# Optimization experiments

Hardware: AMD Instinct MI355X
Metric: run time of the kernel (lower is better)

## Reference

```python
import jax, jax.numpy as jnp
import numpy as np

N, Tq, Tk = 4096, 48, 48
E, H = 64, 4
HD = E // H
TN = 288            # time_num (5-min slots per day)
FE = 4              # forward_expansion
EPS = 1e-5


def _ln(x, g, b):
    mu = jnp.mean(x, axis=-1, keepdims=True)
    var = jnp.var(x, axis=-1, keepdims=True)
    return (x - mu) * jax.lax.rsqrt(var + EPS) * g + b


def setup_inputs() -> dict:
    rng = jax.random.key(0)
    ks = jax.random.split(rng, 12)
    s = 0.05
    return {
        "value": jax.random.normal(ks[0], (N, Tk, E), jnp.float32),
        "keys": jax.random.normal(ks[1], (N, Tk, E), jnp.float32),
        "query": jax.random.normal(ks[2], (N, Tq, E), jnp.float32),
        "Wv": jax.random.normal(ks[3], (HD, HD), jnp.float32) * s,
        "Wk": jax.random.normal(ks[4], (HD, HD), jnp.float32) * s,
        "Wq": jax.random.normal(ks[5], (HD, HD), jnp.float32) * s,
        "Wo": jax.random.normal(ks[6], (E, E), jnp.float32) * s,
        "bo": jnp.zeros((E,), jnp.float32),
        "temb": jax.random.normal(ks[7], (TN, E), jnp.float32) * s,
        "ln1_g": jnp.ones((E,), jnp.float32),
        "ln1_b": jnp.zeros((E,), jnp.float32),
        "ln2_g": jnp.ones((E,), jnp.float32),
        "ln2_b": jnp.zeros((E,), jnp.float32),
        "W1": jax.random.normal(ks[8], (FE * E, E), jnp.float32) * s,  # torch Linear(E, FE*E).weight
        "b1": jnp.zeros((FE * E,), jnp.float32),
        "W2": jax.random.normal(ks[9], (E, FE * E), jnp.float32) * s,
        "b2": jnp.zeros((E,), jnp.float32),
        "tq": 10,
    }


def reference(value, keys, query, Wv, Wk, Wq, Wo, bo, temb,
              ln1_g, ln1_b, ln2_g, ln2_b, W1, b1, W2, b2, tq):
    # temporal embedding add (tk = tq since tk=-1 default)
    tq_inds = (TN + tq + jnp.arange(Tq)) % TN
    tk_inds = (TN + tq + jnp.arange(Tk)) % TN
    q = query + temb[tq_inds][None, :, :]   # (N,Tq,E)
    k = keys + temb[tk_inds][None, :, :]    # (N,Tk,E)

    qh = q.reshape(N, Tq, H, HD)
    kh = k.reshape(N, Tk, H, HD)
    vh = value.reshape(N, Tk, H, HD)
    # per-head small linear projections (x @ W.T, no bias)
    qh = jnp.einsum('nthd,ed->nthe', qh, Wq)
    kh = jnp.einsum('nthd,ed->nthe', kh, Wk)
    vh = jnp.einsum('nthd,ed->nthe', vh, Wv)

    energy = jnp.einsum('nqhd,nkhd->nqkh', qh, kh)  # (N,Tq,Tk,H)
    # causal mask (mask=True path): masked entries set to -1e6 BEFORE scale+clamp
    tmask = jnp.tril(jnp.ones((Tq, Tk), jnp.float32))
    energy = jnp.where(tmask[None, :, :, None] == 0, jnp.float32(-1e6), energy)
    logits = jnp.clip(energy / jnp.float32(np.sqrt(E)), -5.0, 5.0)
    attention = jax.nn.softmax(logits, axis=2)       # softmax over k

    out = jnp.einsum('nqkh,nkhd->nqhd', attention, vh).reshape(N, Tq, E)
    out = out @ Wo.T + bo

    x = _ln(out + q, ln1_g, ln1_b)                   # dropout is identity (eval)
    ff = jax.nn.relu(x @ W1.T + b1) @ W2.T + b2
    return _ln(ff + x, ln2_g, ln2_b)
```

## Files before the change

kernel.cpp:

```cpp
#include <hip/hip_runtime.h>
#include <hip/hip_bf16.h>
#include <math.h>

#define NSEQ 4096
#define TN 288
#define EPSF 1e-5f

typedef short bf16x8 __attribute__((ext_vector_type(8)));
typedef float f32x4 __attribute__((ext_vector_type(4)));

#define WSV 0
#define WSK 256
#define WSQ 512
#define WSO 768
#define WS1 4864
#define WS2 21248

#define A_S   0
#define B_S   3456
#define C_S   6912
#define D_S   10496
#define CD_F  3456
#define H_S   6912

__device__ __forceinline__ unsigned short f2bf_u(float f) {
    __hip_bfloat16 h = __float2bfloat16(f);
    return *reinterpret_cast<const unsigned short*>(&h);
}
__device__ __forceinline__ unsigned int pk2(float a, float b) {
    return (unsigned int)f2bf_u(a) | ((unsigned int)f2bf_u(b) << 16);
}
__device__ __forceinline__ float bits2f(unsigned int u) { return __uint_as_float(u); }
__device__ __forceinline__ float halfsum(float v) {
    v += __shfl_xor(v, 1);
    v += __shfl_xor(v, 2);
    v += __shfl_xor(v, 4);
    v += __shfl_xor(v, 8);
    v += __shfl_xor(v, 16);
    return v;
}

__global__ void wconv_kernel(const float* __restrict__ Wv, const float* __restrict__ Wk,
                             const float* __restrict__ Wq, const float* __restrict__ Wo,
                             const float* __restrict__ W1, const float* __restrict__ W2,
                             short* __restrict__ ws) {
    int i = blockIdx.x * 256 + threadIdx.x;
    float v;
    if (i < 256)        v = Wv[i];
    else if (i < 512)   v = Wk[i - 256];
    else if (i < 768)   v = Wq[i - 512] * 0.125f;
    else if (i < 4864)  v = Wo[i - 768];
    else if (i < 21248) v = W1[i - 4864];
    else                v = W2[i - 21248];
    ws[i] = (short)f2bf_u(v);
}

__global__ __launch_bounds__(256, 5)
void ttrans_kernel(const float* __restrict__ value,
                   const float* __restrict__ keys,
                   const float* __restrict__ query,
                   const float* __restrict__ bo,
                   const float* __restrict__ temb,
                   const float* __restrict__ ln1g,
                   const float* __restrict__ ln1b,
                   const float* __restrict__ ln2g,
                   const float* __restrict__ ln2b,
                   const float* __restrict__ pb1,
                   const float* __restrict__ pb2,
                   const short* __restrict__ ws,
                   const int* __restrict__ tqp,
                   float* __restrict__ out)
{
    __shared__ __align__(16) unsigned char smem[27136];
    short* S16 = reinterpret_cast<short*>(smem);
    float* S32 = reinterpret_cast<float*>(smem);

    const int tid  = threadIdx.x;
    const int lane = tid & 63;
    const int w    = tid >> 6;
    const int l15  = lane & 15;
    const int lg   = lane >> 4;
    const int n    = blockIdx.x;
    const size_t gbase = (size_t)n * 3072;
    const int tqv  = *tqp;
    const int c0   = (lane & 31) * 2;
    const int sub  = lane >> 5;
    const int hh   = w;

    float2 qres2[6];
    {
        int t0 = w * 12 + sub;
        int ti = ((tqv % TN) + TN + t0) % TN;
        #pragma unroll
        for (int it2 = 0; it2 < 6; ++it2) {
            int t = t0 + it2 * 2;
            float2 tv = *reinterpret_cast<const float2*>(&temb[ti * 64 + c0]);
            float2 qv = *reinterpret_cast<const float2*>(&query[gbase + t * 64 + c0]);
            float2 kv = *reinterpret_cast<const float2*>(&keys [gbase + t * 64 + c0]);
            float2 vv = *reinterpret_cast<const float2*>(&value[gbase + t * 64 + c0]);
            float q0 = qv.x + tv.x, q1 = qv.y + tv.y;
            float k0 = kv.x + tv.x, k1 = kv.y + tv.y;
            qres2[it2] = make_float2(q0, q1);
            *reinterpret_cast<unsigned int*>(&S16[A_S + t * 72 + c0]) = pk2(q0, q1);
            *reinterpret_cast<unsigned int*>(&S16[B_S + t * 72 + c0]) = pk2(k0, k1);
            *reinterpret_cast<unsigned int*>(&S16[C_S + t * 72 + c0]) = pk2(vv.x, vv.y);
            ti += 2; if (ti >= TN) ti -= TN;
        }
    }
    __syncthreads();

    {
        bf16x8 bWv = {}, bWk = {}, bWq = {};
        if (lane < 32) {
            bWv = *reinterpret_cast<const bf16x8*>(&ws[WSV + l15 * 16 + lg * 8]);
            bWk = *reinterpret_cast<const bf16x8*>(&ws[WSK + l15 * 16 + lg * 8]);
            bWq = *reinterpret_cast<const bf16x8*>(&ws[WSQ + l15 * 16 + lg * 8]);
        }
        #pragma unroll
        for (int rt = 0; rt < 3; ++rt) {
            bf16x8 aQ = {}, aK = {}, aV = {};
            if (lane < 32) {
                int ro = (rt * 16 + l15) * 72 + hh * 16 + lg * 8;
                aQ = *reinterpret_cast<const bf16x8*>(&S16[A_S + ro]);
                aK = *reinterpret_cast<const bf16x8*>(&S16[B_S + ro]);
                aV = *reinterpret_cast<const bf16x8*>(&S16[C_S + ro]);
            }
            f32x4 z = {0.f,0.f,0.f,0.f};
            f32x4 cQ = __builtin_amdgcn_mfma_f32_16x16x32_bf16(aQ, bWq, z, 0, 0, 0);
            f32x4 cK = __builtin_amdgcn_mfma_f32_16x16x32_bf16(aK, bWk, z, 0, 0, 0);
            f32x4 cV = __builtin_amdgcn_mfma_f32_16x16x32_bf16(aV, bWv, z, 0, 0, 0);
            #pragma unroll
            for (int r = 0; r < 4; ++r) {
                int row = rt * 16 + lg * 4 + r;
                S16[A_S + row * 72 + hh * 16 + l15] = (short)f2bf_u(cQ[r]);
                S16[B_S + row * 72 + hh * 16 + l15] = (short)f2bf_u(cK[r]);
                S16[D_S + (hh * 16 + l15) * 48 + row] = (short)f2bf_u(cV[r]);
            }
        }
    }
    __syncthreads();

    {
        bf16x8 bK0 = {}, bK1 = {}, bK2 = {};
        if (lane < 32) {
            bK0 = *reinterpret_cast<const bf16x8*>(&S16[B_S + ( 0 + l15) * 72 + hh * 16 + lg * 8]);
            bK1 = *reinterpret_cast<const bf16x8*>(&S16[B_S + (16 + l15) * 72 + hh * 16 + lg * 8]);
            bK2 = *reinterpret_cast<const bf16x8*>(&S16[B_S + (32 + l15) * 72 + hh * 16 + lg * 8]);
        }
        bf16x8 vA = *reinterpret_cast<const bf16x8*>(&S16[D_S + (hh * 16 + l15) * 48 + lg * 8]);
        bf16x8 vB = {};
        if (lane < 32)
            vB = *reinterpret_cast<const bf16x8*>(&S16[D_S + (hh * 16 + l15) * 48 + 32 + lg * 8]);

        #pragma unroll
        for (int rt = 0; rt < 3; ++rt) {
            bf16x8 aQ = {};
            if (lane < 32)
                aQ = *reinterpret_cast<const bf16x8*>(&S16[A_S + (rt * 16 + l15) * 72 + hh * 16 + lg * 8]);
            f32x4 z = {0.f,0.f,0.f,0.f};
            f32x4 e0 = __builtin_amdgcn_mfma_f32_16x16x32_bf16(aQ, bK0, z, 0, 0, 0);
            f32x4 e1 = __builtin_amdgcn_mfma_f32_16x16x32_bf16(aQ, bK1, z, 0, 0, 0);
            f32x4 e2 = __builtin_amdgcn_mfma_f32_16x16x32_bf16(aQ, bK2, z, 0, 0, 0);
            #pragma unroll
            for (int r = 0; r < 4; ++r) {
                int t = rt * 16 + lg * 4 + r;
                float v0 = fminf(5.f, fmaxf(-5.f, e0[r]));
                float v1 = fminf(5.f, fmaxf(-5.f, e1[r]));
                float v2 = fminf(5.f, fmaxf(-5.f, e2[r]));
                v0 = ( 0 + l15 <= t) ? v0 : -5.f;
                v1 = (16 + l15 <= t) ? v1 : -5.f;
                v2 = (32 + l15 <= t) ? v2 : -5.f;
                float p0 = __expf(v0), p1 = __expf(v1), p2 = __expf(v2);
                float s = p0 + p1 + p2;
                s += __shfl_xor(s, 1);
                s += __shfl_xor(s, 2);
                s += __shfl_xor(s, 4);
                s += __shfl_xor(s, 8);
                float inv = __builtin_amdgcn_rcpf(s);
                int tl = lg * 4 + r;
                S16[C_S + hh * 896 + tl * 56 +  0 + l15] = (short)f2bf_u(p0 * inv);
                S16[C_S + hh * 896 + tl * 56 + 16 + l15] = (short)f2bf_u(p1 * inv);
                S16[C_S + hh * 896 + tl * 56 + 32 + l15] = (short)f2bf_u(p2 * inv);
            }
            bf16x8 a0 = *reinterpret_cast<const bf16x8*>(&S16[C_S + hh * 896 + l15 * 56 + lg * 8]);
            bf16x8 a1 = {};
            if (lane < 32)
                a1 = *reinterpret_cast<const bf16x8*>(&S16[C_S + hh * 896 + l15 * 56 + 32 + lg * 8]);
            f32x4 zz = {0.f,0.f,0.f,0.f};
            f32x4 oc = __builtin_amdgcn_mfma_f32_16x16x32_bf16(a0, vA, zz, 0, 0, 0);
            oc = __builtin_amdgcn_mfma_f32_16x16x32_bf16(a1, vB, oc, 0, 0, 0);
            #pragma unroll
            for (int r = 0; r < 4; ++r)
                S16[B_S + (rt * 16 + lg * 4 + r) * 72 + hh * 16 + l15] = (short)f2bf_u(oc[r]);
        }
    }
    __syncthreads();

    {
        bf16x8 bO0 = *reinterpret_cast<const bf16x8*>(&ws[WSO + (w * 16 + l15) * 64 + lg * 8]);
        bf16x8 bO1 = *reinterpret_cast<const bf16x8*>(&ws[WSO + (w * 16 + l15) * 64 + 32 + lg * 8]);
        const float bo_v = bo[w * 16 + l15];
        #pragma unroll
        for (int mt = 0; mt < 3; ++mt) {
            bf16x8 a0 = *reinterpret_cast<const bf16x8*>(&S16[B_S + (mt * 16 + l15) * 72 + lg * 8]);
            bf16x8 a1 = *reinterpret_cast<const bf16x8*>(&S16[B_S + (mt * 16 + l15) * 72 + 32 + lg * 8]);
            f32x4 c = {0.f,0.f,0.f,0.f};
            c = __builtin_amdgcn_mfma_f32_16x16x32_bf16(a0, bO0, c, 0, 0, 0);
            c = __builtin_amdgcn_mfma_f32_16x16x32_bf16(a1, bO1, c, 0, 0, 0);
            #pragma unroll
            for (int r = 0; r < 4; ++r)
                S32[CD_F + (mt * 16 + lg * 4 + r) * 68 + w * 16 + l15] = c[r] + bo_v;
        }
    }
    __syncthreads();

    {
        float2 g12  = *reinterpret_cast<const float2*>(&ln1g[c0]);
        float2 be12 = *reinterpret_cast<const float2*>(&ln1b[c0]);
        #pragma unroll
        for (int it2 = 0; it2 < 6; ++it2) {
            int t = w * 12 + it2 * 2 + sub;
            float2 o2 = *reinterpret_cast<const float2*>(&S32[CD_F + t * 68 + c0]);
            float v0 = o2.x + qres2[it2].x;
            float v1 = o2.y + qres2[it2].y;
            float s1 = halfsum(v0 + v1);
            float s2 = halfsum(v0 * v0 + v1 * v1);
            float mu  = s1 * (1.f / 64.f);
            float ex2 = s2 * (1.f / 64.f);
            float var = ex2 - mu * mu;
            float rs = __builtin_amdgcn_rsqf(var + EPSF);
            float x0 = (v0 - mu) * rs * g12.x + be12.x;
            float x1 = (v1 - mu) * rs * g12.y + be12.y;
            *reinterpret_cast<unsigned int*>(&S16[A_S + t * 72 + c0]) = pk2(x0, x1);
        }
    }
    __syncthreads();

    f32x4 ffC[3];
    #pragma unroll
    for (int mt = 0; mt < 3; ++mt) ffC[mt] = (f32x4){0.f,0.f,0.f,0.f};

    #pragma unroll
    for (int hb = 0; hb < 2; ++hb) {
        #pragma unroll
        for (int jj = 0; jj < 2; ++jj) {
            int j16 = w * 2 + jj;
            int jrow = (hb * 8 + j16) * 16 + l15;
            bf16x8 b0 = *reinterpret_cast<const bf16x8*>(&ws[WS1 + jrow * 64 + lg * 8]);
            bf16x8 b1 = *reinterpret_cast<const bf16x8*>(&ws[WS1 + jrow * 64 + 32 + lg * 8]);
            float b1v = pb1[jrow];
            #pragma unroll
            for (int mt = 0; mt < 3; ++mt) {
                bf16x8 a0 = *reinterpret_cast<const bf16x8*>(&S16[A_S + (mt * 16 + l15) * 72 + lg * 8]);
                bf16x8 a1 = *reinterpret_cast<const bf16x8*>(&S16[A_S + (mt * 16 + l15) * 72 + 32 + lg * 8]);
                f32x4 c = {0.f,0.f,0.f,0.f};
                c = __builtin_amdgcn_mfma_f32_16x16x32_bf16(a0, b0, c, 0, 0, 0);
                c = __builtin_amdgcn_mfma_f32_16x16x32_bf16(a1, b1, c, 0, 0, 0);
                #pragma unroll
                for (int r = 0; r < 4; ++r)
                    S16[H_S + (mt * 16 + lg * 4 + r) * 136 + j16 * 16 + l15] =
                        (short)f2bf_u(fmaxf(c[r] + b1v, 0.f));
            }
        }
        __syncthreads();

        {
            const int wb = WS2 + (w * 16 + l15) * 256 + hb * 128;
            bf16x8 bw0 = *reinterpret_cast<const bf16x8*>(&ws[wb +  0 + lg * 8]);
            bf16x8 bw1 = *reinterpret_cast<const bf16x8*>(&ws[wb + 32 + lg * 8]);
            bf16x8 bw2 = *reinterpret_cast<const bf16x8*>(&ws[wb + 64 + lg * 8]);
            bf16x8 bw3 = *reinterpret_cast<const bf16x8*>(&ws[wb + 96 + lg * 8]);
            #pragma unroll
            for (int mt = 0; mt < 3; ++mt) {
                bf16x8 a0 = *reinterpret_cast<const bf16x8*>(&S16[H_S + (mt * 16 + l15) * 136 +  0 + lg * 8]);
                bf16x8 a1 = *reinterpret_cast<const bf16x8*>(&S16[H_S + (mt * 16 + l15) * 136 + 32 + lg * 8]);
                bf16x8 a2 = *reinterpret_cast<const bf16x8*>(&S16[H_S + (mt * 16 + l15) * 136 + 64 + lg * 8]);
                bf16x8 a3 = *reinterpret_cast<const bf16x8*>(&S16[H_S + (mt * 16 + l15) * 136 + 96 + lg * 8]);
                ffC[mt] = __builtin_amdgcn_mfma_f32_16x16x32_bf16(a0, bw0, ffC[mt], 0, 0, 0);
                ffC[mt] = __builtin_amdgcn_mfma_f32_16x16x32_bf16(a1, bw1, ffC[mt], 0, 0, 0);
                ffC[mt] = __builtin_amdgcn_mfma_f32_16x16x32_bf16(a2, bw2, ffC[mt], 0, 0, 0);
                ffC[mt] = __builtin_amdgcn_mfma_f32_16x16x32_bf16(a3, bw3, ffC[mt], 0, 0, 0);
            }
        }
        if (hb == 0) __syncthreads();
    }

    {
        float b2v = pb2[w * 16 + l15];
        #pragma unroll
        for (int mt = 0; mt < 3; ++mt)
            #pragma unroll
            for (int r = 0; r < 4; ++r)
                S16[B_S + (mt * 16 + lg * 4 + r) * 72 + w * 16 + l15] =
                    (short)f2bf_u(ffC[mt][r] + b2v);
    }
    __syncthreads();

    {
        float2 g22  = *reinterpret_cast<const float2*>(&ln2g[c0]);
        float2 be22 = *reinterpret_cast<const float2*>(&ln2b[c0]);
        #pragma unroll
        for (int it2 = 0; it2 < 6; ++it2) {
            int t = w * 12 + it2 * 2 + sub;
            unsigned int fp = *reinterpret_cast<const unsigned int*>(&S16[B_S + t * 72 + c0]);
            unsigned int xp = *reinterpret_cast<const unsigned int*>(&S16[A_S + t * 72 + c0]);
            float v0 = bits2f(fp << 16) + bits2f(xp << 16);
            float v1 = bits2f(fp & 0xffff0000u) + bits2f(xp & 0xffff0000u);
            float s1 = halfsum(v0 + v1);
            float s2 = halfsum(v0 * v0 + v1 * v1);
            float mu  = s1 * (1.f / 64.f);
            float ex2 = s2 * (1.f / 64.f);
            float var = ex2 - mu * mu;
            float rs = __builtin_amdgcn_rsqf(var + EPSF);
            float y0 = (v0 - mu) * rs * g22.x + be22.x;
            float y1 = (v1 - mu) * rs * g22.y + be22.y;
            *reinterpret_cast<float2*>(&out[gbase + t * 64 + c0]) = make_float2(y0, y1);
        }
    }
}

extern "C" void kernel_launch(void* const* d_in, const int* in_sizes, int n_in,
                              void* d_out, int out_size, void* d_ws, size_t ws_size,
                              hipStream_t stream) {
    const float* value = (const float*)d_in[0];
    const float* keys  = (const float*)d_in[1];
    const float* query = (const float*)d_in[2];
    const float* Wv    = (const float*)d_in[3];
    const float* Wk    = (const float*)d_in[4];
    const float* Wq    = (const float*)d_in[5];
    const float* Wo    = (const float*)d_in[6];
    const float* bo    = (const float*)d_in[7];
    const float* temb  = (const float*)d_in[8];
    const float* ln1g  = (const float*)d_in[9];
    const float* ln1b  = (const float*)d_in[10];
    const float* ln2g  = (const float*)d_in[11];
    const float* ln2b  = (const float*)d_in[12];
    const float* W1    = (const float*)d_in[13];
    const float* b1    = (const float*)d_in[14];
    const float* W2    = (const float*)d_in[15];
    const float* b2    = (const float*)d_in[16];
    const int*   tq    = (const int*)d_in[17];
    float* outp = (float*)d_out;
    short* ws = (short*)d_ws;

    hipLaunchKernelGGL(wconv_kernel, dim3(147), dim3(256), 0, stream,
                       Wv, Wk, Wq, Wo, W1, W2, ws);
    hipLaunchKernelGGL(ttrans_kernel, dim3(NSEQ), dim3(256), 0, stream,
                       value, keys, query, bo, temb,
                       ln1g, ln1b, ln2g, ln2b, b1, b2, ws, tq, outp);
}
```

Before: 91.86 us.

## Skip fully-masked QK tiles and compute softmax row sums via MFMA

```diff
diff --git a/kernel.cpp b/kernel.cpp
--- a/kernel.cpp
+++ b/kernel.cpp
@@ -141,6 +141,10 @@
     __syncthreads();
 
     {
+        const unsigned short PBF = f2bf_u(0.006737946999085467f);
+        bf16x8 ones;
+        #pragma unroll
+        for (int i = 0; i < 8; ++i) ones[i] = (short)0x3F80;
         bf16x8 bK0 = {}, bK1 = {}, bK2 = {};
         if (lane < 32) {
             bK0 = *reinterpret_cast<const bf16x8*>(&S16[B_S + ( 0 + l15) * 72 + hh * 16 + lg * 8]);
@@ -159,39 +163,45 @@
                 aQ = *reinterpret_cast<const bf16x8*>(&S16[A_S + (rt * 16 + l15) * 72 + hh * 16 + lg * 8]);
             f32x4 z = {0.f,0.f,0.f,0.f};
             f32x4 e0 = __builtin_amdgcn_mfma_f32_16x16x32_bf16(aQ, bK0, z, 0, 0, 0);
-            f32x4 e1 = __builtin_amdgcn_mfma_f32_16x16x32_bf16(aQ, bK1, z, 0, 0, 0);
-            f32x4 e2 = __builtin_amdgcn_mfma_f32_16x16x32_bf16(aQ, bK2, z, 0, 0, 0);
+            f32x4 e1 = z, e2 = z;
+            if (rt >= 1) e1 = __builtin_amdgcn_mfma_f32_16x16x32_bf16(aQ, bK1, z, 0, 0, 0);
+            if (rt == 2) e2 = __builtin_amdgcn_mfma_f32_16x16x32_bf16(aQ, bK2, z, 0, 0, 0);
+            const int abase = C_S + hh * 896;
             #pragma unroll
             for (int r = 0; r < 4; ++r) {
-                int t = rt * 16 + lg * 4 + r;
+                int tl = lg * 4 + r;
+                int t = rt * 16 + tl;
                 float v0 = fminf(5.f, fmaxf(-5.f, e0[r]));
-                float v1 = fminf(5.f, fmaxf(-5.f, e1[r]));
-                float v2 = fminf(5.f, fmaxf(-5.f, e2[r]));
-                v0 = ( 0 + l15 <= t) ? v0 : -5.f;
-                v1 = (16 + l15 <= t) ? v1 : -5.f;
-                v2 = (32 + l15 <= t) ? v2 : -5.f;
-                float p0 = __expf(v0), p1 = __expf(v1), p2 = __expf(v2);
-                float s = p0 + p1 + p2;
-                s += __shfl_xor(s, 1);
-                s += __shfl_xor(s, 2);
-                s += __shfl_xor(s, 4);
-                s += __shfl_xor(s, 8);
-                float inv = __builtin_amdgcn_rcpf(s);
-                int tl = lg * 4 + r;
-                S16[C_S + hh * 896 + tl * 56 +  0 + l15] = (short)f2bf_u(p0 * inv);
-                S16[C_S + hh * 896 + tl * 56 + 16 + l15] = (short)f2bf_u(p1 * inv);
-                S16[C_S + hh * 896 + tl * 56 + 32 + l15] = (short)f2bf_u(p2 * inv);
-            }
-            bf16x8 a0 = *reinterpret_cast<const bf16x8*>(&S16[C_S + hh * 896 + l15 * 56 + lg * 8]);
+                if (rt == 0) v0 = (l15 <= t) ? v0 : -5.f;
+                S16[abase + tl * 56 + l15] = (short)f2bf_u(__expf(v0));
+                if (rt == 0) {
+                    S16[abase + tl * 56 + 16 + l15] = (short)PBF;
+                } else {
+                    float v1 = fminf(5.f, fmaxf(-5.f, e1[r]));
+                    if (rt == 1) v1 = (16 + l15 <= t) ? v1 : -5.f;
+                    S16[abase + tl * 56 + 16 + l15] = (short)f2bf_u(__expf(v1));
+                }
+                if (rt < 2) {
+                    S16[abase + tl * 56 + 32 + l15] = (short)PBF;
+                } else {
+                    float v2 = fminf(5.f, fmaxf(-5.f, e2[r]));
+                    v2 = (32 + l15 <= t) ? v2 : -5.f;
+                    S16[abase + tl * 56 + 32 + l15] = (short)f2bf_u(__expf(v2));
+                }
+            }
+            bf16x8 a0 = *reinterpret_cast<const bf16x8*>(&S16[abase + l15 * 56 + lg * 8]);
             bf16x8 a1 = {};
             if (lane < 32)
-                a1 = *reinterpret_cast<const bf16x8*>(&S16[C_S + hh * 896 + l15 * 56 + 32 + lg * 8]);
-            f32x4 zz = {0.f,0.f,0.f,0.f};
-            f32x4 oc = __builtin_amdgcn_mfma_f32_16x16x32_bf16(a0, vA, zz, 0, 0, 0);
+                a1 = *reinterpret_cast<const bf16x8*>(&S16[abase + l15 * 56 + 32 + lg * 8]);
+            f32x4 sc = __builtin_amdgcn_mfma_f32_16x16x32_bf16(a0, ones, z, 0, 0, 0);
+            sc = __builtin_amdgcn_mfma_f32_16x16x32_bf16(a1, ones, sc, 0, 0, 0);
+            f32x4 oc = __builtin_amdgcn_mfma_f32_16x16x32_bf16(a0, vA, z, 0, 0, 0);
             oc = __builtin_amdgcn_mfma_f32_16x16x32_bf16(a1, vB, oc, 0, 0, 0);
             #pragma unroll
-            for (int r = 0; r < 4; ++r)
-                S16[B_S + (rt * 16 + lg * 4 + r) * 72 + hh * 16 + l15] = (short)f2bf_u(oc[r]);
+            for (int r = 0; r < 4; ++r) {
+                float ov = oc[r] * __builtin_amdgcn_rcpf(sc[r]);
+                S16[B_S + (rt * 16 + lg * 4 + r) * 72 + hh * 16 + l15] = (short)f2bf_u(ov);
+            }
         }
     }
     __syncthreads();
```

Result: slower. 96.32 us (+4.9%).
